# Kernel optimization log

Hardware: AMD Instinct MI355X
Metric: run time of the kernel (lower is better)

Reference implementation:

```python
import jax, jax.numpy as jnp
import numpy as np

F = 256  # filters
FQ = F // 8  # query/key channels


def setup_inputs() -> dict:
    key = jax.random.key(0)
    ks = jax.random.split(key, 9)
    B, H, W = 4, 64, 64
    s_in = 1.0 / np.sqrt(F)
    inp = {
        "inputs": jax.random.normal(ks[0], (B, H, W, F), jnp.float32),
        "Wq": jax.random.normal(ks[1], (F, FQ), jnp.float32) * s_in,
        "bq": jnp.zeros((FQ,), jnp.float32),
        "Wk": jax.random.normal(ks[2], (F, FQ), jnp.float32) * s_in,
        "bk": jnp.zeros((FQ,), jnp.float32),
        "Wv": jax.random.normal(ks[3], (F, F), jnp.float32) * s_in,
        "bv": jnp.zeros((F,), jnp.float32),
        "Wo": jax.random.normal(ks[4], (F, F), jnp.float32) * s_in,
        "bo": jnp.zeros((F,), jnp.float32),
    }
    return inp


def reference(inputs, Wq, bq, Wk, bk, Wv, bv, Wo, bo):
    B, H, W, C = inputs.shape
    N = H * W
    x = inputs.reshape(B, N, C)  # 1x1 conv == per-token linear
    q = jax.nn.relu(jnp.einsum('bnc,cd->bnd', x, Wq) + bq)  # [B,N,FQ]
    k = jax.nn.relu(jnp.einsum('bnc,cd->bnd', x, Wk) + bk)  # [B,N,FQ]
    v = jax.nn.relu(jnp.einsum('bnc,cd->bnd', x, Wv) + bv)  # [B,N,C]
    # unscaled full attention (as in the original module)
    attn = jax.nn.softmax(jnp.einsum('bnd,bmd->bnm', q, k), axis=-1)  # [B,N,N]
    attended = jnp.einsum('bnm,bmc->bnc', attn, v)  # [B,N,C]
    out = jax.nn.relu(jnp.einsum('bnc,cd->bnd', attended, Wo) + bo)
    return inputs + out.reshape(B, H, W, C)
```

## Files before the change

kernel.cpp:

```cpp
#include <hip/hip_runtime.h>

typedef __attribute__((ext_vector_type(8))) short short8;
typedef __attribute__((ext_vector_type(4))) float floatx4;
typedef __attribute__((ext_vector_type(2))) unsigned int uintx2;
typedef __attribute__((ext_vector_type(4))) unsigned int uintx4;

#define MFMA16(a, b, c) __builtin_amdgcn_mfma_f32_16x16x32_bf16((a), (b), (c), 0, 0, 0)

#define LDP 72
#define LDO 264
#define LOG2E 1.4426950408889634f
#define PSHIFT 23.083120654223414f

__device__ __forceinline__ float bf2f(unsigned short u) {
  return __uint_as_float(((unsigned int)u) << 16);
}
__device__ __forceinline__ unsigned short f2bf(float f) {
  unsigned int x = __float_as_uint(f);
  x += 0x7FFFu + ((x >> 16) & 1u);
  return (unsigned short)(x >> 16);
}
__device__ __forceinline__ unsigned int cvt_pk_bf16(float lo, float hi) {
  unsigned int r;
  asm("v_cvt_pk_bf16_f32 %0, %1, %2" : "=v"(r) : "v"(lo), "v"(hi));
  return r;
}
__device__ __forceinline__ float ld_in(const void* p, long i, int isf32) {
  if (isf32) return ((const float*)p)[i];
  return bf2f(((const unsigned short*)p)[i]);
}
__device__ __forceinline__ short8 ld16(const unsigned short* p) {
  return *(const short8*)__builtin_assume_aligned(p, 16);
}
__device__ __forceinline__ void st16(unsigned short* p, short8 v) {
  *(short8*)__builtin_assume_aligned(p, 16) = v;
}
__device__ __forceinline__ int detect_bad(const unsigned short* x, int idx) {
  const short8 v = ld16(x + (long)idx * 8);
  int bad = 0;
#pragma unroll
  for (int j = 0; j < 8; j++) {
    const unsigned int e = (((unsigned short)v[j]) >> 7) & 0xFFu;
    if (e >= 141u) bad = 1;
  }
  return bad;
}


__global__ __launch_bounds__(256)
void prep_kernel(const void* __restrict__ x,
                 const void* __restrict__ Wq, const void* __restrict__ Wk,
                 const void* __restrict__ Wv, const void* __restrict__ Wo,
                 unsigned short* __restrict__ Wf_qk,
                 unsigned short* __restrict__ Wf_v,
                 unsigned short* __restrict__ Wf_o) {
  __shared__ unsigned short Vl[64][LDP];
  __shared__ int flagl[4];
  const int t = (int)threadIdx.x;
  const int wave = t >> 6, lane = t & 63;
  {
    const int bad = detect_bad((const unsigned short*)x, t) |
                    detect_bad((const unsigned short*)x, 256 + t);
    if (lane == 0) flagl[wave] = (__ballot(bad) != 0ull) ? 1 : 0;
  }
  __syncthreads();
  const int isf32 = flagl[0] | flagl[1] | flagl[2] | flagl[3];

  const int blk = (int)blockIdx.x;
  const int j = t & 63, r4 = t >> 6;

  if (blk < 32) {
    const void* W = (blk < 16) ? Wo : Wv;
    unsigned short* dst = (blk < 16) ? Wf_o : Wf_v;
    const int b2 = blk & 15;
    const int g0 = (b2 >> 2) * 64, c0 = (b2 & 3) * 64;
#pragma unroll
    for (int k2 = 0; k2 < 16; k2++) {
      const int rr = r4 * 16 + k2;
      Vl[j][rr] = f2bf(ld_in(W, (long)(c0 + rr) * 256 + g0 + j, isf32));
    }
    __syncthreads();
#pragma unroll
    for (int cc = 0; cc < 2; cc++) {
      const int c = t + cc * 256;
      const int f_l = c >> 6, lane_c = c & 63;
      const int og = f_l >> 1, kse = f_l & 1;
      const int out_l = lane_c & 15, q = lane_c >> 4;
      const short8 v = ld16(&Vl[og * 16 + out_l][kse * 32 + q * 8]);
      st16(dst + (long)(((g0 >> 4) + og) * 8 + (c0 >> 5) + kse) * 512 + lane_c * 8, v);
    }
  } else {
    const int c0 = (blk - 32) * 64;
#pragma unroll
    for (int k2 = 0; k2 < 16; k2++) {
      const int cl = r4 * 16 + k2;
      const float v = (j < 32) ? ld_in(Wq, (long)(c0 + cl) * 32 + j, isf32) * LOG2E
                               : ld_in(Wk, (long)(c0 + cl) * 32 + (j - 32), isf32);
      Vl[j][cl] = f2bf(v);
    }
    __syncthreads();
#pragma unroll
    for (int cc = 0; cc < 2; cc++) {
      const int c = t + cc * 256;
      const int f_l = c >> 6, lane_c = c & 63;
      const int og = f_l >> 1, kse = f_l & 1;
      const int out_l = lane_c & 15, q = lane_c >> 4;
      const short8 v = ld16(&Vl[og * 16 + out_l][kse * 32 + q * 8]);
      st16(Wf_qk + (long)(og * 8 + (c0 >> 5) + kse) * 512 + lane_c * 8, v);
    }
  }
}

__global__ __launch_bounds__(256)
void proj_kernel(const void* __restrict__ x,
                 const void* __restrict__ bq, const void* __restrict__ bk,
                 const void* __restrict__ bv,
                 const unsigned short* __restrict__ Wf_qk,
                 const unsigned short* __restrict__ Wf_v,
                 unsigned short* __restrict__ Qf, unsigned short* __restrict__ Kf,
                 unsigned short* __restrict__ Vf) {
  __shared__ unsigned short Vl[64][LDP];
  __shared__ int flagl[4];
  const int t = (int)threadIdx.x;
  const int wave = t >> 6, lane = t & 63, quad = lane >> 4, l15 = lane & 15;

  {
    const int bad = detect_bad((const unsigned short*)x, t) |
                    detect_bad((const unsigned short*)x, 256 + t);
    if (lane == 0) flagl[wave] = (__ballot(bad) != 0ull) ? 1 : 0;
  }
  __syncthreads();
  const int isf32 = flagl[0] | flagl[1] | flagl[2] | flagl[3];

  const int blk = (int)blockIdx.x;
  const int ct = blk % 5;
  const long row_base = (long)(blk / 5) * 64;
  const long arow = row_base + wave * 16 + l15;

  const unsigned short* wb = (ct == 0) ? Wf_qk
                                       : (Wf_v + (long)(ct - 1) * 4 * 8 * 512);

  floatx4 acc[4];
  acc[0] = acc[1] = acc[2] = acc[3] = (floatx4)0.0f;

#pragma unroll
  for (int ks = 0; ks < 8; ks++) {
    short8 a;
    if (isf32) {
      const float* xf = (const float*)x + arow * 256 + ks * 32 + quad * 8;
      const floatx4 f0 = *(const floatx4*)xf;
      const floatx4 f1 = *(const floatx4*)(xf + 4);
      uintx4 u;
      u[0] = cvt_pk_bf16(f0[0], f0[1]); u[1] = cvt_pk_bf16(f0[2], f0[3]);
      u[2] = cvt_pk_bf16(f1[0], f1[1]); u[3] = cvt_pk_bf16(f1[2], f1[3]);
      a = *(short8*)&u;
    } else {
      a = ld16((const unsigned short*)x + arow * 256 + ks * 32 + quad * 8);
    }
#pragma unroll
    for (int tn = 0; tn < 4; tn++) {
      const short8 bfr = ld16(wb + (long)(tn * 8 + ks) * 512 + lane * 8);
      acc[tn] = MFMA16(a, bfr, acc[tn]);
    }
  }

  if (ct == 0) {
#pragma unroll
    for (int tn = 0; tn < 4; tn++) {
      const int g = tn * 16 + l15;
      const float bias = (g < 32) ? ld_in(bq, g, isf32) * LOG2E
                                  : ld_in(bk, g - 32, isf32);
#pragma unroll
      for (int r = 0; r < 4; r++)
        Vl[wave * 16 + quad * 4 + r][g] = f2bf(fmaxf(acc[tn][r] + bias, 0.0f));
    }
    __syncthreads();
    const long f0 = row_base >> 4;
#pragma unroll
    for (int cc = 0; cc < 2; cc++) {
      const int c = t + cc * 256;
      const int isK = c >> 8;
      const int c2 = c & 255;
      const int f_l = c2 >> 6, lane_c = c2 & 63;
      const int row_l = lane_c & 15, q = lane_c >> 4;
      const short8 v = ld16(&Vl[f_l * 16 + row_l][isK * 32 + q * 8]);
      unsigned short* dst = isK ? Kf : Qf;
      st16(dst + (f0 + f_l) * 512 + lane_c * 8, v);
    }
  } else {
#pragma unroll
    for (int tn = 0; tn < 4; tn++) {
      const float bias = ld_in(bv, (long)(ct - 1) * 64 + tn * 16 + l15, isf32);
#pragma unroll
      for (int r = 0; r < 4; r++)
        Vl[tn * 16 + l15][wave * 16 + quad * 4 + r] =
            f2bf(fmaxf(acc[tn][r] + bias, 0.0f));
    }
    __syncthreads();
    const long bb = row_base >> 12;
    const int kt = (int)((row_base & 4095) >> 6);
    const long fbase = (bb * 64 + kt) * 32 + (long)(ct - 1) * 8;
#pragma unroll
    for (int cc = 0; cc < 2; cc++) {
      const int c = t * 2 + cc;
      const int f_l = c >> 6, lane_c = c & 63;
      const int cg = f_l >> 1, kh = f_l & 1;
      const int ch_l = lane_c & 15, q = lane_c >> 4;
      const short8 v = ld16(&Vl[cg * 16 + ch_l][kh * 32 + q * 8]);
      st16(Vf + (fbase + f_l) * 512 + lane_c * 8, v);
    }
  }
}

__global__ __launch_bounds__(512, 2)
void flash_kernel(const unsigned short* __restrict__ Qf,
                  const unsigned short* __restrict__ Kf,
                  const unsigned short* __restrict__ Vf,
                  const unsigned short* __restrict__ Wf_o,
                  const void* __restrict__ bo,
                  const void* __restrict__ xin, void* __restrict__ out) {
  __shared__ unsigned short Pl[2][64 * LDP];
  __shared__ unsigned short Ol[64 * LDO];
  __shared__ float Lp[2][64];
  __shared__ float Ll[64];
  __shared__ int flagl[8];

  const int t = (int)threadIdx.x;
  const int wave = t >> 6, lane = t & 63, quad = lane >> 4, l15 = lane & 15;

  {
    const int bad = detect_bad((const unsigned short*)xin, t);
    if (lane == 0) flagl[wave] = (__ballot(bad) != 0ull) ? 1 : 0;
  }

  const int raw = (int)blockIdx.x;
  const int b = raw & 3;
  const int mt = raw >> 2;
  const long qrow0 = (long)b * 4096 + (long)mt * 64;
  const int m = wave & 3, h = wave >> 2;

  const long kfrag0 = (long)b * 256;
  const long vfrag0 = (long)b * 64 * 32;

  const short8 qf = ld16(Qf + ((qrow0 >> 4) + m) * 512 + lane * 8);

  floatx4 oacc[4][2];
#pragma unroll
  for (int i = 0; i < 4; i++) { oacc[i][0] = (floatx4)0.0f; oacc[i][1] = (floatx4)0.0f; }
  float lpart = 0.0f;

  short8 kb[2];
#pragma unroll
  for (int i = 0; i < 2; i++)
    kb[i] = ld16(Kf + (kfrag0 + h * 2 + i) * 512 + lane * 8);
  {
    floatx4 s[2];
#pragma unroll
    for (int i = 0; i < 2; i++) { s[i] = (floatx4)0.0f; s[i] = MFMA16(kb[i], qf, s[i]); }
    unsigned short* pl = Pl[0];
#pragma unroll
    for (int i = 0; i < 2; i++) {
      const float p0 = exp2f(s[i][0] - PSHIFT);
      const float p1 = exp2f(s[i][1] - PSHIFT);
      const float p2 = exp2f(s[i][2] - PSHIFT);
      const float p3 = exp2f(s[i][3] - PSHIFT);
      lpart += (p0 + p1) + (p2 + p3);
      uintx2 w;
      w[0] = cvt_pk_bf16(p0, p1);
      w[1] = cvt_pk_bf16(p2, p3);
      *(uintx2*)__builtin_assume_aligned(
          &pl[(m * 16 + l15) * LDP + h * 32 + i * 16 + quad * 4], 8) = w;
    }
  }
#pragma unroll
  for (int i = 0; i < 2; i++)
    kb[i] = ld16(Kf + (kfrag0 + 4 + h * 2 + i) * 512 + lane * 8);
  __syncthreads();

  for (int kt = 0; kt < 64; kt++) {
    short8 vb[2][2];
#pragma unroll
    for (int tv = 0; tv < 2; tv++)
#pragma unroll
      for (int kh = 0; kh < 2; kh++)
        vb[tv][kh] = ld16(Vf + (vfrag0 + (long)kt * 32 + (wave * 2 + tv) * 2 + kh) * 512 + lane * 8);

    const unsigned short* plr = Pl[kt & 1];
    short8 pa[4][2];
#pragma unroll
    for (int rm = 0; rm < 4; rm++)
#pragma unroll
      for (int kh = 0; kh < 2; kh++)
        pa[rm][kh] = ld16(&plr[(rm * 16 + l15) * LDP + kh * 32 + quad * 8]);

    short8 kbn[2];
    const int kt2 = (kt + 2) & 63;
#pragma unroll
    for (int i = 0; i < 2; i++)
      kbn[i] = ld16(Kf + (kfrag0 + kt2 * 4 + h * 2 + i) * 512 + lane * 8);

    if (kt < 63) {
      floatx4 s[2];
#pragma unroll
      for (int i = 0; i < 2; i++) { s[i] = (floatx4)0.0f; s[i] = MFMA16(kb[i], qf, s[i]); }
      unsigned short* pl = Pl[(kt + 1) & 1];
#pragma unroll
      for (int i = 0; i < 2; i++) {
        const float p0 = exp2f(s[i][0] - PSHIFT);
        const float p1 = exp2f(s[i][1] - PSHIFT);
        const float p2 = exp2f(s[i][2] - PSHIFT);
        const float p3 = exp2f(s[i][3] - PSHIFT);
        lpart += (p0 + p1) + (p2 + p3);
        uintx2 w;
        w[0] = cvt_pk_bf16(p0, p1);
        w[1] = cvt_pk_bf16(p2, p3);
        *(uintx2*)__builtin_assume_aligned(
            &pl[(m * 16 + l15) * LDP + h * 32 + i * 16 + quad * 4], 8) = w;
      }
    }
    kb[0] = kbn[0]; kb[1] = kbn[1];

    __builtin_amdgcn_s_setprio(1);
#pragma unroll
    for (int kh = 0; kh < 2; kh++)
#pragma unroll
      for (int tv = 0; tv < 2; tv++)
#pragma unroll
        for (int rm = 0; rm < 4; rm++)
          oacc[rm][tv] = MFMA16(pa[rm][kh], vb[tv][kh], oacc[rm][tv]);
    __builtin_amdgcn_s_setprio(0);
    __syncthreads();
  }

  lpart += __shfl_xor(lpart, 16);
  lpart += __shfl_xor(lpart, 32);
  if (lane < 16) Lp[h][m * 16 + lane] = lpart;
  __syncthreads();
  if (t < 64) Ll[t] = 1.0f / (Lp[0][t] + Lp[1][t]);
  __syncthreads();

#pragma unroll
  for (int rm = 0; rm < 4; rm++) {
    const floatx4 ll = *(const floatx4*)&Ll[rm * 16 + quad * 4];
#pragma unroll
    for (int tv = 0; tv < 2; tv++)
#pragma unroll
      for (int r = 0; r < 4; r++)
        Ol[(rm * 16 + quad * 4 + r) * LDO + wave * 32 + tv * 16 + l15] =
            f2bf(oacc[rm][tv][r] * ll[r]);
  }
  __syncthreads();

  const int isf32 = flagl[0] | flagl[1] | flagl[2] | flagl[3] |
                    flagl[4] | flagl[5] | flagl[6] | flagl[7];
  const int m2 = wave & 3, gh = wave >> 2;
  floatx4 acc2[8];
#pragma unroll
  for (int i = 0; i < 8; i++) acc2[i] = (floatx4)0.0f;
#pragma unroll
  for (int ks = 0; ks < 8; ks++) {
    const short8 a = ld16(&Ol[(m2 * 16 + l15) * LDO + ks * 32 + quad * 8]);
#pragma unroll
    for (int tn = 0; tn < 8; tn++) {
      const short8 bfr = ld16(Wf_o + (long)((gh * 8 + tn) * 8 + ks) * 512 + lane * 8);
      acc2[tn] = MFMA16(a, bfr, acc2[tn]);
    }
  }
  __syncthreads();
#pragma unroll
  for (int tn = 0; tn < 8; tn++) {
    const int g = gh * 128 + tn * 16 + l15;
    const float bias = ld_in(bo, g, isf32);
#pragma unroll
    for (int r = 0; r < 4; r++)
      Ol[(m2 * 16 + quad * 4 + r) * LDO + g] = f2bf(fmaxf(acc2[tn][r] + bias, 0.0f));
  }
  __syncthreads();

  if (isf32) {
    const float* xf = (const float*)xin + qrow0 * 256;
    float* of = (float*)out + qrow0 * 256;
#pragma unroll
    for (int p = 0; p < 8; p++) {
      const int idx = p * 2048 + t * 4;
      const int row = idx >> 8, ch = idx & 255;
      floatx4 xv = *(const floatx4*)(xf + idx);
      floatx4 ov;
#pragma unroll
      for (int j = 0; j < 4; j++) ov[j] = bf2f(Ol[row * LDO + ch + j]) + xv[j];
      *(floatx4*)(of + idx) = ov;
    }
  } else {
    const unsigned short* xh = (const unsigned short*)xin + qrow0 * 256;
    unsigned short* oh = (unsigned short*)out + qrow0 * 256;
#pragma unroll
    for (int p = 0; p < 4; p++) {
      const int idx = p * 4096 + t * 8;
      const int row = idx >> 8, ch = idx & 255;
      const short8 xv = ld16(xh + idx);
      short8 ov;
#pragma unroll
      for (int j = 0; j < 8; j++)
        ov[j] = (short)f2bf(bf2f(Ol[row * LDO + ch + j]) + bf2f((unsigned short)xv[j]));
      st16(oh + idx, ov);
    }
  }
}

extern "C" void kernel_launch(void* const* d_in, const int* in_sizes, int n_in,
                              void* d_out, int out_size, void* d_ws, size_t ws_size,
                              hipStream_t stream) {
  const void* x  = d_in[0];
  const void* Wq = d_in[1]; const void* bq = d_in[2];
  const void* Wk = d_in[3]; const void* bk = d_in[4];
  const void* Wv = d_in[5]; const void* bv = d_in[6];
  const void* Wo = d_in[7]; const void* bo = d_in[8];

  char* ws = (char*)d_ws;
  unsigned short* Qf    = (unsigned short*)ws;
  unsigned short* Kf    = Qf + (long)4 * 4096 * 32;
  unsigned short* Vf    = Kf + (long)4 * 4096 * 32;
  unsigned short* Wf_o  = Vf + (long)4 * 256 * 4096;
  unsigned short* Wf_v  = Wf_o + (long)128 * 512;
  unsigned short* Wf_qk = Wf_v + (long)128 * 512;

  prep_kernel<<<36, 256, 0, stream>>>(x, Wq, Wk, Wv, Wo, Wf_qk, Wf_v, Wf_o);
  proj_kernel<<<1280, 256, 0, stream>>>(x, bq, bk, bv, Wf_qk, Wf_v, Qf, Kf, Vf);
  flash_kernel<<<256, 512, 0, stream>>>(Qf, Kf, Vf, Wf_o, bo, x, d_out);
}
```

Before: 166.5 us.

## Compute all QKV column tiles per row block in one proj_kernel workgroup

Each proj_kernel workgroup now handles all five output column groups (QK plus four V groups) for its 64 rows, instead of launching five workgroups per row block. The x tile is loaded and converted once and reused across 20 accumulator tiles, which cuts redundant input reads and the repeated format-detection work. The cost is five times fewer workgroups (256), higher register pressure from 80 accumulator floats per lane, and extra syncs between the five epilogue passes. LDP padding also changes from 72 to 80, which alters the shared-memory layout used by the flash kernel as well.

```diff
diff --git a/kernel.cpp b/kernel.cpp
--- a/kernel.cpp
+++ b/kernel.cpp
@@ -7,7 +7,7 @@
 
 #define MFMA16(a, b, c) __builtin_amdgcn_mfma_f32_16x16x32_bf16((a), (b), (c), 0, 0, 0)
 
-#define LDP 72
+#define LDP 80
 #define LDO 264
 #define LOG2E 1.4426950408889634f
 #define PSHIFT 23.083120654223414f
@@ -111,7 +111,7 @@
   }
 }
 
-__global__ __launch_bounds__(256)
+__global__ __launch_bounds__(256, 1)
 void proj_kernel(const void* __restrict__ x,
                  const void* __restrict__ bq, const void* __restrict__ bk,
                  const void* __restrict__ bv,
@@ -132,16 +132,12 @@
   __syncthreads();
   const int isf32 = flagl[0] | flagl[1] | flagl[2] | flagl[3];
 
-  const int blk = (int)blockIdx.x;
-  const int ct = blk % 5;
-  const long row_base = (long)(blk / 5) * 64;
+  const long row_base = (long)blockIdx.x * 64;
   const long arow = row_base + wave * 16 + l15;
 
-  const unsigned short* wb = (ct == 0) ? Wf_qk
-                                       : (Wf_v + (long)(ct - 1) * 4 * 8 * 512);
-
-  floatx4 acc[4];
-  acc[0] = acc[1] = acc[2] = acc[3] = (floatx4)0.0f;
+  floatx4 acc[20];
+#pragma unroll
+  for (int i = 0; i < 20; i++) acc[i] = (floatx4)0.0f;
 
 #pragma unroll
   for (int ks = 0; ks < 8; ks++) {
@@ -158,57 +154,65 @@
       a = ld16((const unsigned short*)x + arow * 256 + ks * 32 + quad * 8);
     }
 #pragma unroll
-    for (int tn = 0; tn < 4; tn++) {
-      const short8 bfr = ld16(wb + (long)(tn * 8 + ks) * 512 + lane * 8);
-      acc[tn] = MFMA16(a, bfr, acc[tn]);
-    }
-  }
-
-  if (ct == 0) {
-#pragma unroll
-    for (int tn = 0; tn < 4; tn++) {
-      const int g = tn * 16 + l15;
-      const float bias = (g < 32) ? ld_in(bq, g, isf32) * LOG2E
-                                  : ld_in(bk, g - 32, isf32);
-#pragma unroll
-      for (int r = 0; r < 4; r++)
-        Vl[wave * 16 + quad * 4 + r][g] = f2bf(fmaxf(acc[tn][r] + bias, 0.0f));
-    }
-    __syncthreads();
-    const long f0 = row_base >> 4;
-#pragma unroll
-    for (int cc = 0; cc < 2; cc++) {
-      const int c = t + cc * 256;
-      const int isK = c >> 8;
-      const int c2 = c & 255;
-      const int f_l = c2 >> 6, lane_c = c2 & 63;
-      const int row_l = lane_c & 15, q = lane_c >> 4;
-      const short8 v = ld16(&Vl[f_l * 16 + row_l][isK * 32 + q * 8]);
-      unsigned short* dst = isK ? Kf : Qf;
-      st16(dst + (f0 + f_l) * 512 + lane_c * 8, v);
-    }
-  } else {
-#pragma unroll
-    for (int tn = 0; tn < 4; tn++) {
-      const float bias = ld_in(bv, (long)(ct - 1) * 64 + tn * 16 + l15, isf32);
-#pragma unroll
-      for (int r = 0; r < 4; r++)
-        Vl[tn * 16 + l15][wave * 16 + quad * 4 + r] =
-            f2bf(fmaxf(acc[tn][r] + bias, 0.0f));
-    }
-    __syncthreads();
-    const long bb = row_base >> 12;
-    const int kt = (int)((row_base & 4095) >> 6);
-    const long fbase = (bb * 64 + kt) * 32 + (long)(ct - 1) * 8;
-#pragma unroll
-    for (int cc = 0; cc < 2; cc++) {
-      const int c = t * 2 + cc;
-      const int f_l = c >> 6, lane_c = c & 63;
-      const int cg = f_l >> 1, kh = f_l & 1;
-      const int ch_l = lane_c & 15, q = lane_c >> 4;
-      const short8 v = ld16(&Vl[cg * 16 + ch_l][kh * 32 + q * 8]);
-      st16(Vf + (fbase + f_l) * 512 + lane_c * 8, v);
-    }
+    for (int g = 0; g < 5; g++)
+#pragma unroll
+      for (int tn = 0; tn < 4; tn++) {
+        const unsigned short* wptr =
+            (g == 0) ? (Wf_qk + (long)(tn * 8 + ks) * 512)
+                     : (Wf_v + (long)(((g - 1) * 4 + tn) * 8 + ks) * 512);
+        acc[g * 4 + tn] = MFMA16(a, ld16(wptr + lane * 8), acc[g * 4 + tn]);
+      }
+  }
+
+#pragma unroll
+  for (int g = 0; g < 5; g++) {
+    if (g == 0) {
+#pragma unroll
+      for (int tn = 0; tn < 4; tn++) {
+        const int gcol = tn * 16 + l15;
+        const float bias = (gcol < 32) ? ld_in(bq, gcol, isf32) * LOG2E
+                                       : ld_in(bk, gcol - 32, isf32);
+#pragma unroll
+        for (int r = 0; r < 4; r++)
+          Vl[wave * 16 + quad * 4 + r][gcol] = f2bf(fmaxf(acc[tn][r] + bias, 0.0f));
+      }
+      __syncthreads();
+      const long f0 = row_base >> 4;
+#pragma unroll
+      for (int cc = 0; cc < 2; cc++) {
+        const int c = t + cc * 256;
+        const int isK = c >> 8;
+        const int c2 = c & 255;
+        const int f_l = c2 >> 6, lane_c = c2 & 63;
+        const int row_l = lane_c & 15, q = lane_c >> 4;
+        const short8 v = ld16(&Vl[f_l * 16 + row_l][isK * 32 + q * 8]);
+        unsigned short* dst = isK ? Kf : Qf;
+        st16(dst + (f0 + f_l) * 512 + lane_c * 8, v);
+      }
+    } else {
+#pragma unroll
+      for (int tn = 0; tn < 4; tn++) {
+        const float bias = ld_in(bv, (long)(g - 1) * 64 + tn * 16 + l15, isf32);
+#pragma unroll
+        for (int r = 0; r < 4; r++)
+          Vl[tn * 16 + l15][wave * 16 + quad * 4 + r] =
+              f2bf(fmaxf(acc[g * 4 + tn][r] + bias, 0.0f));
+      }
+      __syncthreads();
+      const long bb = row_base >> 12;
+      const int kt = (int)((row_base & 4095) >> 6);
+      const long fbase = (bb * 64 + kt) * 32 + (long)(g - 1) * 8;
+#pragma unroll
+      for (int cc = 0; cc < 2; cc++) {
+        const int c = t * 2 + cc;
+        const int f_l = c >> 6, lane_c = c & 63;
+        const int cg = f_l >> 1, kh = f_l & 1;
+        const int ch_l = lane_c & 15, q = lane_c >> 4;
+        const short8 v = ld16(&Vl[cg * 16 + ch_l][kh * 32 + q * 8]);
+        st16(Vf + (fbase + f_l) * 512 + lane_c * 8, v);
+      }
+    }
+    if (g < 4) __syncthreads();
   }
 }
 
@@ -425,6 +429,6 @@
   unsigned short* Wf_qk = Wf_v + (long)128 * 512;
 
   prep_kernel<<<36, 256, 0, stream>>>(x, Wq, Wk, Wv, Wo, Wf_qk, Wf_v, Wf_o);
-  proj_kernel<<<1280, 256, 0, stream>>>(x, bq, bk, bv, Wf_qk, Wf_v, Qf, Kf, Vf);
+  proj_kernel<<<256, 256, 0, stream>>>(x, bq, bk, bv, Wf_qk, Wf_v, Qf, Kf, Vf);
   flash_kernel<<<256, 512, 0, stream>>>(Qf, Kf, Vf, Wf_o, bo, x, d_out);
 }
```

New measurement: 195.9 us. 17.7% more time.

## Process two key tiles per flash iteration with quad-buffered P in LDS

Applied to the files above, without the earlier changes.

The flash loop now handles two 64-key tiles per iteration with four P buffers, which halves the number of block-wide barriers and gives the scheduler more independent MFMA and load work between syncs. The P row padding changes from 72 to 80 to alter the LDS bank mapping. The projection kernel's block-to-tile mapping changes from mod-5 to shift/mask. In exchange, register pressure rises from doubled V, P and K fragments, and LDS use grows, which may limit occupancy at two blocks of 512 threads.

```diff
diff --git a/kernel.cpp b/kernel.cpp
--- a/kernel.cpp
+++ b/kernel.cpp
@@ -7,7 +7,7 @@
 
 #define MFMA16(a, b, c) __builtin_amdgcn_mfma_f32_16x16x32_bf16((a), (b), (c), 0, 0, 0)
 
-#define LDP 72
+#define LDP 80
 #define LDO 264
 #define LOG2E 1.4426950408889634f
 #define PSHIFT 23.083120654223414f
@@ -133,8 +133,8 @@
   const int isf32 = flagl[0] | flagl[1] | flagl[2] | flagl[3];
 
   const int blk = (int)blockIdx.x;
-  const int ct = blk % 5;
-  const long row_base = (long)(blk / 5) * 64;
+  const int ct = blk >> 8;
+  const long row_base = (long)(blk & 255) * 64;
   const long arow = row_base + wave * 16 + l15;
 
   const unsigned short* wb = (ct == 0) ? Wf_qk
@@ -219,7 +219,7 @@
                   const unsigned short* __restrict__ Wf_o,
                   const void* __restrict__ bo,
                   const void* __restrict__ xin, void* __restrict__ out) {
-  __shared__ unsigned short Pl[2][64 * LDP];
+  __shared__ unsigned short Pl[4][64 * LDP];
   __shared__ unsigned short Ol[64 * LDO];
   __shared__ float Lp[2][64];
   __shared__ float Ll[64];
@@ -249,15 +249,18 @@
   for (int i = 0; i < 4; i++) { oacc[i][0] = (floatx4)0.0f; oacc[i][1] = (floatx4)0.0f; }
   float lpart = 0.0f;
 
-  short8 kb[2];
-#pragma unroll
-  for (int i = 0; i < 2; i++)
-    kb[i] = ld16(Kf + (kfrag0 + h * 2 + i) * 512 + lane * 8);
-  {
+  short8 kb[2][2];
+#pragma unroll
+  for (int j = 0; j < 2; j++)
+#pragma unroll
+    for (int i = 0; i < 2; i++)
+      kb[j][i] = ld16(Kf + (kfrag0 + j * 4 + h * 2 + i) * 512 + lane * 8);
+#pragma unroll
+  for (int j = 0; j < 2; j++) {
     floatx4 s[2];
 #pragma unroll
-    for (int i = 0; i < 2; i++) { s[i] = (floatx4)0.0f; s[i] = MFMA16(kb[i], qf, s[i]); }
-    unsigned short* pl = Pl[0];
+    for (int i = 0; i < 2; i++) { s[i] = (floatx4)0.0f; s[i] = MFMA16(kb[j][i], qf, s[i]); }
+    unsigned short* pl = Pl[j];
 #pragma unroll
     for (int i = 0; i < 2; i++) {
       const float p0 = exp2f(s[i][0] - PSHIFT);
@@ -273,61 +276,82 @@
     }
   }
 #pragma unroll
-  for (int i = 0; i < 2; i++)
-    kb[i] = ld16(Kf + (kfrag0 + 4 + h * 2 + i) * 512 + lane * 8);
-  __syncthreads();
-
-  for (int kt = 0; kt < 64; kt++) {
-    short8 vb[2][2];
-#pragma unroll
-    for (int tv = 0; tv < 2; tv++)
+  for (int j = 0; j < 2; j++)
+#pragma unroll
+    for (int i = 0; i < 2; i++)
+      kb[j][i] = ld16(Kf + (kfrag0 + (2 + j) * 4 + h * 2 + i) * 512 + lane * 8);
+  __syncthreads();
+
+  for (int it = 0; it < 32; it++) {
+    const int t0 = 2 * it;
+    const int rb = (it & 1) * 2;
+    const int wb2 = 2 - rb;
+
+    short8 vb[2][2][2];
+#pragma unroll
+    for (int j = 0; j < 2; j++)
+#pragma unroll
+      for (int tv = 0; tv < 2; tv++)
+#pragma unroll
+        for (int kh = 0; kh < 2; kh++)
+          vb[j][tv][kh] = ld16(Vf + (vfrag0 + (long)(t0 + j) * 32 +
+                                     (wave * 2 + tv) * 2 + kh) * 512 + lane * 8);
+
+    short8 pa[2][4][2];
+#pragma unroll
+    for (int j = 0; j < 2; j++) {
+      const unsigned short* plr = Pl[rb + j];
+#pragma unroll
+      for (int rm = 0; rm < 4; rm++)
+#pragma unroll
+        for (int kh = 0; kh < 2; kh++)
+          pa[j][rm][kh] = ld16(&plr[(rm * 16 + l15) * LDP + kh * 32 + quad * 8]);
+    }
+
+    short8 kbn[2][2];
+#pragma unroll
+    for (int j = 0; j < 2; j++) {
+      const int ktp = (t0 + 4 + j) & 63;
+#pragma unroll
+      for (int i = 0; i < 2; i++)
+        kbn[j][i] = ld16(Kf + (kfrag0 + ktp * 4 + h * 2 + i) * 512 + lane * 8);
+    }
+
+    if (it < 31) {
+#pragma unroll
+      for (int j = 0; j < 2; j++) {
+        floatx4 s[2];
+#pragma unroll
+        for (int i = 0; i < 2; i++) { s[i] = (floatx4)0.0f; s[i] = MFMA16(kb[j][i], qf, s[i]); }
+        unsigned short* pl = Pl[wb2 + j];
+#pragma unroll
+        for (int i = 0; i < 2; i++) {
+          const float p0 = exp2f(s[i][0] - PSHIFT);
+          const float p1 = exp2f(s[i][1] - PSHIFT);
+          const float p2 = exp2f(s[i][2] - PSHIFT);
+          const float p3 = exp2f(s[i][3] - PSHIFT);
+          lpart += (p0 + p1) + (p2 + p3);
+          uintx2 w;
+          w[0] = cvt_pk_bf16(p0, p1);
+          w[1] = cvt_pk_bf16(p2, p3);
+          *(uintx2*)__builtin_assume_aligned(
+              &pl[(m * 16 + l15) * LDP + h * 32 + i * 16 + quad * 4], 8) = w;
+        }
+      }
+    }
+#pragma unroll
+    for (int j = 0; j < 2; j++) { kb[j][0] = kbn[j][0]; kb[j][1] = kbn[j][1]; }
+
+    __builtin_amdgcn_s_setprio(1);
+#pragma unroll
+    for (int j = 0; j < 2; j++)
 #pragma unroll
       for (int kh = 0; kh < 2; kh++)
-        vb[tv][kh] = ld16(Vf + (vfrag0 + (long)kt * 32 + (wave * 2 + tv) * 2 + kh) * 512 + lane * 8);
-
-    const unsigned short* plr = Pl[kt & 1];
-    short8 pa[4][2];
-#pragma unroll
-    for (int rm = 0; rm < 4; rm++)
-#pragma unroll
-      for (int kh = 0; kh < 2; kh++)
-        pa[rm][kh] = ld16(&plr[(rm * 16 + l15) * LDP + kh * 32 + quad * 8]);
-
-    short8 kbn[2];
-    const int kt2 = (kt + 2) & 63;
-#pragma unroll
-    for (int i = 0; i < 2; i++)
-      kbn[i] = ld16(Kf + (kfrag0 + kt2 * 4 + h * 2 + i) * 512 + lane * 8);
-
-    if (kt < 63) {
-      floatx4 s[2];
-#pragma unroll
-      for (int i = 0; i < 2; i++) { s[i] = (floatx4)0.0f; s[i] = MFMA16(kb[i], qf, s[i]); }
-      unsigned short* pl = Pl[(kt + 1) & 1];
-#pragma unroll
-      for (int i = 0; i < 2; i++) {
-        const float p0 = exp2f(s[i][0] - PSHIFT);
-        const float p1 = exp2f(s[i][1] - PSHIFT);
-        const float p2 = exp2f(s[i][2] - PSHIFT);
-        const float p3 = exp2f(s[i][3] - PSHIFT);
-        lpart += (p0 + p1) + (p2 + p3);
-        uintx2 w;
-        w[0] = cvt_pk_bf16(p0, p1);
-        w[1] = cvt_pk_bf16(p2, p3);
-        *(uintx2*)__builtin_assume_aligned(
-            &pl[(m * 16 + l15) * LDP + h * 32 + i * 16 + quad * 4], 8) = w;
-      }
-    }
-    kb[0] = kbn[0]; kb[1] = kbn[1];
-
-    __builtin_amdgcn_s_setprio(1);
-#pragma unroll
-    for (int kh = 0; kh < 2; kh++)
-#pragma unroll
-      for (int tv = 0; tv < 2; tv++)
-#pragma unroll
-        for (int rm = 0; rm < 4; rm++)
-          oacc[rm][tv] = MFMA16(pa[rm][kh], vb[tv][kh], oacc[rm][tv]);
+#pragma unroll
+        for (int tv = 0; tv < 2; tv++)
+#pragma unroll
+          for (int rm = 0; rm < 4; rm++)
+            oacc[rm][tv] = MFMA16(pa[j][rm][kh], vb[j][tv][kh], oacc[rm][tv]);
     __builtin_amdgcn_s_setprio(0);
     __syncthreads();
   }
```

Result: no change. 168.5 us (+1.2%).
